# Kernel tuning notes

Measured on AMD Instinct MI355X. Metric: run time of the kernel, lower is better.

Reference implementation:

```python
import jax, jax.numpy as jnp
import numpy as np

N_USERS = 200000
N_ITEMS = 200000
HOPS = 4      # n_hops + 1
DIM = 64
BATCH = 2048
N_NEGS = 64
K = 2
DECAY = 1e-4


def setup_inputs() -> dict:
    key = jax.random.key(0)
    k1, k2, k3, k4, k5, k6 = jax.random.split(key, 6)
    return {
        "user_gcn_emb": jax.random.normal(k1, (N_USERS, HOPS, DIM), dtype=jnp.float32),
        "item_gcn_emb": jax.random.normal(k2, (N_ITEMS, HOPS, DIM), dtype=jnp.float32),
        "seed_embed": jax.random.normal(k3, (BATCH, 1), dtype=jnp.float32),
        "user": jax.random.randint(k4, (BATCH,), 0, N_USERS, dtype=jnp.int64 if jax.config.jax_enable_x64 else jnp.int32),
        "pos_item": jax.random.randint(k5, (BATCH,), 0, N_ITEMS, dtype=jnp.int64 if jax.config.jax_enable_x64 else jnp.int32),
        "neg_item": jax.random.randint(k6, (BATCH, K * N_NEGS), 0, N_ITEMS, dtype=jnp.int64 if jax.config.jax_enable_x64 else jnp.int32),
    }


def _negative_sampling(user_gcn_emb, item_gcn_emb, user, neg_candidates, pos_item, seed_embed):
    # s_e, p_e: [B, H, C]; n_e: [B, N, H, C]
    s_e = user_gcn_emb[user]
    p_e = item_gcn_emb[pos_item]
    n_e = item_gcn_emb[neg_candidates]
    seed = seed_embed[:, :, None, None]                      # [B,1,1,1]
    # positive mixing
    n_e_ = seed * p_e[:, None, :, :] + (1.0 - seed) * n_e    # [B,N,H,C]
    # hop mixing: per-hop inner product scores
    scores = jnp.einsum("bhc,bnhc->bnh", s_e, n_e_)          # [B,N,H]
    idx = jnp.argmax(scores, axis=1)                         # [B,H] (detached/int)
    # select per-hop hardest mixed negative
    sel = jnp.take_along_axis(n_e_, idx[:, None, :, None], axis=1)  # [B,1,H,C]
    return sel[:, 0]                                         # [B,H,C]


def _bpr_loss(user_e, pos_e_hops, neg_e_hops):
    # user_e/pos_e_hops: [B,H,C]; neg_e_hops: [B,K,H,C]
    B = user_e.shape[0]
    u_e = jnp.mean(user_e, axis=1)          # [B,C]  (pool='mean')
    pos_e = jnp.mean(pos_e_hops, axis=1)    # [B,C]
    neg_e = jnp.mean(neg_e_hops, axis=2)    # [B,K,C]
    pos_scores = jnp.sum(u_e * pos_e, axis=-1)              # [B]
    neg_scores = jnp.einsum("bc,bkc->bk", u_e, neg_e)       # [B,K]
    mf_loss = jnp.mean(jnp.log1p(jnp.sum(jnp.exp(neg_scores - pos_scores[:, None]), axis=1)))
    regularize = (jnp.sum(u_e ** 2) + jnp.sum(pos_e ** 2) + jnp.sum(neg_e ** 2)) / 2.0
    emb_loss = DECAY * regularize / B
    return mf_loss + emb_loss, mf_loss, emb_loss


def reference(user_gcn_emb, item_gcn_emb, seed_embed, user, pos_item, neg_item):
    negs = []
    for k in range(K):
        negs.append(_negative_sampling(
            user_gcn_emb, item_gcn_emb, user,
            neg_item[:, k * N_NEGS:(k + 1) * N_NEGS], pos_item, seed_embed))
    neg_gcn_embs = jnp.stack(negs, axis=1)  # [B,K,H,C]
    loss, mf_loss, emb_loss = _bpr_loss(user_gcn_emb[user], item_gcn_emb[pos_item], neg_gcn_embs)
    return loss, mf_loss, emb_loss
```

## Files before the change

kernel.cpp:

```cpp
#include <hip/hip_runtime.h>
#include <math.h>

#define N_USERS 200000
#define N_ITEMS 200000
#define HOPS 4
#define DIM 64
#define BATCH 2048
#define N_NEGS 64
#define KK 2
#define ROW 256
#define DECAY 0.0001f

__global__ __launch_bounds__(256, 4) void mixgcf_main(
    const float* __restrict__ user_emb,
    const float* __restrict__ item_emb,
    const float* __restrict__ seed_embed,
    const int*   __restrict__ user,
    const int*   __restrict__ pos_item,
    const int*   __restrict__ neg_item,
    float*       __restrict__ ws)
{
    const int b    = blockIdx.x;
    const int tid  = threadIdx.x;
    const int w    = tid >> 6;
    const int lane = tid & 63;

    __shared__ float s_lds[ROW];
    __shared__ float p_lds[ROW];
    __shared__ int   nidx[KK * N_NEGS];
    __shared__ float selv[KK][ROW];
    __shared__ float scw[4][HOPS];

    const int   uidx = user[b];
    const int   pidx = pos_item[b];
    const float seed = seed_embed[b];

    if (tid < 64) {
        ((float4*)s_lds)[tid] = *(const float4*)(user_emb + (size_t)uidx * ROW + tid * 4);
    } else if (tid < 128) {
        ((float4*)p_lds)[tid - 64] = *(const float4*)(item_emb + (size_t)pidx * ROW + (tid - 64) * 4);
    } else {
        nidx[tid - 128] = neg_item[(size_t)b * (KK * N_NEGS) + (tid - 128)];
    }
    __syncthreads();

    const float4 s4 = *(const float4*)(s_lds + lane * 4);
    const float4 p4 = *(const float4*)(p_lds + lane * 4);
    const float  omse = 1.0f - seed;
    const float4 sp = make_float4(seed * p4.x, seed * p4.y, seed * p4.z, seed * p4.w);
    const int h = lane >> 4;

    for (int k = 0; k < KK; ++k) {
        float  best = -INFINITY;
        float4 bv   = make_float4(0.f, 0.f, 0.f, 0.f);

        #pragma unroll 4
        for (int i = 0; i < 16; ++i) {
            const int n  = (i << 2) + w;
            const int it = nidx[k * N_NEGS + n];
            const float4 ne = *(const float4*)(item_emb + (size_t)it * ROW + lane * 4);
            float4 ne_;
            ne_.x = fmaf(omse, ne.x, sp.x);
            ne_.y = fmaf(omse, ne.y, sp.y);
            ne_.z = fmaf(omse, ne.z, sp.z);
            ne_.w = fmaf(omse, ne.w, sp.w);
            float sc = ne_.x * s4.x;
            sc = fmaf(ne_.y, s4.y, sc);
            sc = fmaf(ne_.z, s4.z, sc);
            sc = fmaf(ne_.w, s4.w, sc);
            sc += __shfl_xor(sc, 1);
            sc += __shfl_xor(sc, 2);
            sc += __shfl_xor(sc, 4);
            sc += __shfl_xor(sc, 8);
            if (sc > best) { best = sc; bv = ne_; }
        }

        if ((lane & 15) == 0) scw[w][h] = best;
        __syncthreads();
        float m0 = scw[0][h], m1 = scw[1][h], m2 = scw[2][h], m3 = scw[3][h];
        int winner = 0; float mb = m0;
        if (m1 > mb) { mb = m1; winner = 1; }
        if (m2 > mb) { mb = m2; winner = 2; }
        if (m3 > mb) { mb = m3; winner = 3; }
        if (w == winner) {
            *(float4*)(&selv[k][lane * 4]) = bv;
        }
        __syncthreads();
    }

    if (w == 0) {
        const int c = lane;
        const float ue = 0.25f * (s_lds[c] + s_lds[64 + c] + s_lds[128 + c] + s_lds[192 + c]);
        const float pe = 0.25f * (p_lds[c] + p_lds[64 + c] + p_lds[128 + c] + p_lds[192 + c]);
        const float n0 = 0.25f * (selv[0][c] + selv[0][64 + c] + selv[0][128 + c] + selv[0][192 + c]);
        const float n1 = 0.25f * (selv[1][c] + selv[1][64 + c] + selv[1][128 + c] + selv[1][192 + c]);
        float ps  = ue * pe;
        float ns0 = ue * n0;
        float ns1 = ue * n1;
        float rg  = ue * ue + pe * pe + n0 * n0 + n1 * n1;
        #pragma unroll
        for (int m = 1; m < 64; m <<= 1) {
            ps  += __shfl_xor(ps,  m);
            ns0 += __shfl_xor(ns0, m);
            ns1 += __shfl_xor(ns1, m);
            rg  += __shfl_xor(rg,  m);
        }
        if (lane == 0) {
            const float mf = log1pf(expf(ns0 - ps) + expf(ns1 - ps));
            ws[b]         = mf;
            ws[BATCH + b] = rg;
        }
    }
}

__global__ __launch_bounds__(256) void mixgcf_reduce(const float* __restrict__ ws,
                                                     float* __restrict__ out)
{
    __shared__ float smf[256];
    __shared__ float srg[256];
    const int t = threadIdx.x;
    float mf = 0.f, rg = 0.f;
    for (int i = t; i < BATCH; i += 256) {
        mf += ws[i];
        rg += ws[BATCH + i];
    }
    smf[t] = mf; srg[t] = rg;
    __syncthreads();
    for (int s = 128; s > 0; s >>= 1) {
        if (t < s) { smf[t] += smf[t + s]; srg[t] += srg[t + s]; }
        __syncthreads();
    }
    if (t == 0) {
        const float mf_loss  = smf[0] / (float)BATCH;
        const float emb_loss = DECAY * (srg[0] * 0.5f) / (float)BATCH;
        out[0] = mf_loss + emb_loss;
        out[1] = mf_loss;
        out[2] = emb_loss;
    }
}

extern "C" void kernel_launch(void* const* d_in, const int* in_sizes, int n_in,
                              void* d_out, int out_size, void* d_ws, size_t ws_size,
                              hipStream_t stream)
{
    const float* user_emb  = (const float*)d_in[0];
    const float* item_emb  = (const float*)d_in[1];
    const float* seed      = (const float*)d_in[2];
    const int*   user      = (const int*)d_in[3];
    const int*   pos_item  = (const int*)d_in[4];
    const int*   neg_item  = (const int*)d_in[5];
    float* ws  = (float*)d_ws;
    float* out = (float*)d_out;

    mixgcf_main<<<BATCH, 256, 0, stream>>>(user_emb, item_emb, seed,
                                           user, pos_item, neg_item, ws);
    mixgcf_reduce<<<1, 256, 0, stream>>>(ws, out);
}
```

Before: 50.16 us.

## Fuse final reduction via last-block atomic and interleave both negative groups

The separate reduce kernel is folded into the main kernel: each block bumps an atomic counter, and the last block to finish sums the per-sample partials and writes the losses. A memset resets the counter before each launch. The two K negative groups are now processed in one loop, which issues twice as many independent gathers per iteration and removes a pair of barriers. The user and positive rows are loaded straight from global memory rather than staged through LDS. The cost is an extra memset call plus atomic and fence overhead in every block.

```diff
diff --git a/kernel.cpp b/kernel.cpp
--- a/kernel.cpp
+++ b/kernel.cpp
@@ -11,6 +11,8 @@
 #define ROW 256
 #define DECAY 0.0001f
 
+#define WS_OFF 16
+
 __global__ __launch_bounds__(256, 4) void mixgcf_main(
     const float* __restrict__ user_emb,
     const float* __restrict__ item_emb,
@@ -18,80 +20,91 @@
     const int*   __restrict__ user,
     const int*   __restrict__ pos_item,
     const int*   __restrict__ neg_item,
-    float*       __restrict__ ws)
+    float*       __restrict__ ws,
+    float*       __restrict__ out)
 {
     const int b    = blockIdx.x;
     const int tid  = threadIdx.x;
     const int w    = tid >> 6;
     const int lane = tid & 63;
 
-    __shared__ float s_lds[ROW];
-    __shared__ float p_lds[ROW];
     __shared__ int   nidx[KK * N_NEGS];
     __shared__ float selv[KK][ROW];
-    __shared__ float scw[4][HOPS];
+    __shared__ float scw[KK][4][HOPS];
+    __shared__ float red_mf[256];
+    __shared__ float red_rg[256];
+    __shared__ int   last_flag;
 
     const int   uidx = user[b];
     const int   pidx = pos_item[b];
     const float seed = seed_embed[b];
 
-    if (tid < 64) {
-        ((float4*)s_lds)[tid] = *(const float4*)(user_emb + (size_t)uidx * ROW + tid * 4);
-    } else if (tid < 128) {
-        ((float4*)p_lds)[tid - 64] = *(const float4*)(item_emb + (size_t)pidx * ROW + (tid - 64) * 4);
-    } else {
-        nidx[tid - 128] = neg_item[(size_t)b * (KK * N_NEGS) + (tid - 128)];
-    }
+    if (tid < KK * N_NEGS) nidx[tid] = neg_item[(size_t)b * (KK * N_NEGS) + tid];
     __syncthreads();
 
-    const float4 s4 = *(const float4*)(s_lds + lane * 4);
-    const float4 p4 = *(const float4*)(p_lds + lane * 4);
+    const float4 s4 = *(const float4*)(user_emb + (size_t)uidx * ROW + lane * 4);
+    const float4 p4 = *(const float4*)(item_emb + (size_t)pidx * ROW + lane * 4);
     const float  omse = 1.0f - seed;
     const float4 sp = make_float4(seed * p4.x, seed * p4.y, seed * p4.z, seed * p4.w);
     const int h = lane >> 4;
 
-    for (int k = 0; k < KK; ++k) {
-        float  best = -INFINITY;
-        float4 bv   = make_float4(0.f, 0.f, 0.f, 0.f);
+    float  best0 = -INFINITY, best1 = -INFINITY;
+    float4 bv0 = make_float4(0.f, 0.f, 0.f, 0.f);
+    float4 bv1 = make_float4(0.f, 0.f, 0.f, 0.f);
 
-        #pragma unroll 4
-        for (int i = 0; i < 16; ++i) {
-            const int n  = (i << 2) + w;
-            const int it = nidx[k * N_NEGS + n];
-            const float4 ne = *(const float4*)(item_emb + (size_t)it * ROW + lane * 4);
-            float4 ne_;
-            ne_.x = fmaf(omse, ne.x, sp.x);
-            ne_.y = fmaf(omse, ne.y, sp.y);
-            ne_.z = fmaf(omse, ne.z, sp.z);
-            ne_.w = fmaf(omse, ne.w, sp.w);
-            float sc = ne_.x * s4.x;
-            sc = fmaf(ne_.y, s4.y, sc);
-            sc = fmaf(ne_.z, s4.z, sc);
-            sc = fmaf(ne_.w, s4.w, sc);
-            sc += __shfl_xor(sc, 1);
-            sc += __shfl_xor(sc, 2);
-            sc += __shfl_xor(sc, 4);
-            sc += __shfl_xor(sc, 8);
-            if (sc > best) { best = sc; bv = ne_; }
-        }
+    #pragma unroll 8
+    for (int i = 0; i < 16; ++i) {
+        const int n   = (i << 2) + w;
+        const int it0 = nidx[n];
+        const int it1 = nidx[N_NEGS + n];
+        const float4 ne0 = *(const float4*)(item_emb + (size_t)it0 * ROW + lane * 4);
+        const float4 ne1 = *(const float4*)(item_emb + (size_t)it1 * ROW + lane * 4);
 
-        if ((lane & 15) == 0) scw[w][h] = best;
-        __syncthreads();
-        float m0 = scw[0][h], m1 = scw[1][h], m2 = scw[2][h], m3 = scw[3][h];
-        int winner = 0; float mb = m0;
-        if (m1 > mb) { mb = m1; winner = 1; }
-        if (m2 > mb) { mb = m2; winner = 2; }
-        if (m3 > mb) { mb = m3; winner = 3; }
-        if (w == winner) {
-            *(float4*)(&selv[k][lane * 4]) = bv;
-        }
-        __syncthreads();
+        float4 m0, m1;
+        m0.x = fmaf(omse, ne0.x, sp.x); m1.x = fmaf(omse, ne1.x, sp.x);
+        m0.y = fmaf(omse, ne0.y, sp.y); m1.y = fmaf(omse, ne1.y, sp.y);
+        m0.z = fmaf(omse, ne0.z, sp.z); m1.z = fmaf(omse, ne1.z, sp.z);
+        m0.w = fmaf(omse, ne0.w, sp.w); m1.w = fmaf(omse, ne1.w, sp.w);
+
+        float sc0 = m0.x * s4.x;  float sc1 = m1.x * s4.x;
+        sc0 = fmaf(m0.y, s4.y, sc0); sc1 = fmaf(m1.y, s4.y, sc1);
+        sc0 = fmaf(m0.z, s4.z, sc0); sc1 = fmaf(m1.z, s4.z, sc1);
+        sc0 = fmaf(m0.w, s4.w, sc0); sc1 = fmaf(m1.w, s4.w, sc1);
+
+        sc0 += __shfl_xor(sc0, 1);  sc1 += __shfl_xor(sc1, 1);
+        sc0 += __shfl_xor(sc0, 2);  sc1 += __shfl_xor(sc1, 2);
+        sc0 += __shfl_xor(sc0, 4);  sc1 += __shfl_xor(sc1, 4);
+        sc0 += __shfl_xor(sc0, 8);  sc1 += __shfl_xor(sc1, 8);
+
+        if (sc0 > best0) { best0 = sc0; bv0 = m0; }
+        if (sc1 > best1) { best1 = sc1; bv1 = m1; }
     }
+
+    if ((lane & 15) == 0) { scw[0][w][h] = best0; scw[1][w][h] = best1; }
+    __syncthreads();
+    {
+        float a0 = scw[0][0][h], a1 = scw[0][1][h], a2 = scw[0][2][h], a3 = scw[0][3][h];
+        int win0 = 0; float mb = a0;
+        if (a1 > mb) { mb = a1; win0 = 1; }
+        if (a2 > mb) { mb = a2; win0 = 2; }
+        if (a3 > mb) { mb = a3; win0 = 3; }
+        if (w == win0) *(float4*)(&selv[0][lane * 4]) = bv0;
+
+        float c0 = scw[1][0][h], c1 = scw[1][1][h], c2 = scw[1][2][h], c3 = scw[1][3][h];
+        int win1 = 0; float nb = c0;
+        if (c1 > nb) { nb = c1; win1 = 1; }
+        if (c2 > nb) { nb = c2; win1 = 2; }
+        if (c3 > nb) { nb = c3; win1 = 3; }
+        if (w == win1) *(float4*)(&selv[1][lane * 4]) = bv1;
+    }
+    __syncthreads();
 
     if (w == 0) {
         const int c = lane;
-        const float ue = 0.25f * (s_lds[c] + s_lds[64 + c] + s_lds[128 + c] + s_lds[192 + c]);
-        const float pe = 0.25f * (p_lds[c] + p_lds[64 + c] + p_lds[128 + c] + p_lds[192 + c]);
+        const float* ur = user_emb + (size_t)uidx * ROW;
+        const float* pr = item_emb + (size_t)pidx * ROW;
+        const float ue = 0.25f * (ur[c] + ur[64 + c] + ur[128 + c] + ur[192 + c]);
+        const float pe = 0.25f * (pr[c] + pr[64 + c] + pr[128 + c] + pr[192 + c]);
         const float n0 = 0.25f * (selv[0][c] + selv[0][64 + c] + selv[0][128 + c] + selv[0][192 + c]);
         const float n1 = 0.25f * (selv[1][c] + selv[1][64 + c] + selv[1][128 + c] + selv[1][192 + c]);
         float ps  = ue * pe;
@@ -107,35 +120,37 @@
         }
         if (lane == 0) {
             const float mf = log1pf(expf(ns0 - ps) + expf(ns1 - ps));
-            ws[b]         = mf;
-            ws[BATCH + b] = rg;
+            ws[WS_OFF + b]         = mf;
+            ws[WS_OFF + BATCH + b] = rg;
         }
     }
-}
 
-__global__ __launch_bounds__(256) void mixgcf_reduce(const float* __restrict__ ws,
-                                                     float* __restrict__ out)
-{
-    __shared__ float smf[256];
-    __shared__ float srg[256];
-    const int t = threadIdx.x;
-    float mf = 0.f, rg = 0.f;
-    for (int i = t; i < BATCH; i += 256) {
-        mf += ws[i];
-        rg += ws[BATCH + i];
+    if (tid == 0) {
+        __threadfence();
+        unsigned t = atomicAdd((unsigned*)ws, 1u);
+        last_flag = (t == (unsigned)(BATCH - 1));
     }
-    smf[t] = mf; srg[t] = rg;
     __syncthreads();
-    for (int s = 128; s > 0; s >>= 1) {
-        if (t < s) { smf[t] += smf[t + s]; srg[t] += srg[t + s]; }
+    if (last_flag) {
+        __threadfence();
+        float mf = 0.f, rg = 0.f;
+        for (int i = tid; i < BATCH; i += 256) {
+            mf += ws[WS_OFF + i];
+            rg += ws[WS_OFF + BATCH + i];
+        }
+        red_mf[tid] = mf; red_rg[tid] = rg;
         __syncthreads();
-    }
-    if (t == 0) {
-        const float mf_loss  = smf[0] / (float)BATCH;
-        const float emb_loss = DECAY * (srg[0] * 0.5f) / (float)BATCH;
-        out[0] = mf_loss + emb_loss;
-        out[1] = mf_loss;
-        out[2] = emb_loss;
+        for (int s = 128; s > 0; s >>= 1) {
+            if (tid < s) { red_mf[tid] += red_mf[tid + s]; red_rg[tid] += red_rg[tid + s]; }
+            __syncthreads();
+        }
+        if (tid == 0) {
+            const float mf_loss  = red_mf[0] / (float)BATCH;
+            const float emb_loss = DECAY * (red_rg[0] * 0.5f) / (float)BATCH;
+            out[0] = mf_loss + emb_loss;
+            out[1] = mf_loss;
+            out[2] = emb_loss;
+        }
     }
 }
 
@@ -152,7 +167,7 @@
     float* ws  = (float*)d_ws;
     float* out = (float*)d_out;
 
+    hipMemsetAsync(d_ws, 0, 4, stream);
     mixgcf_main<<<BATCH, 256, 0, stream>>>(user_emb, item_emb, seed,
-                                           user, pos_item, neg_item, ws);
-    mixgcf_reduce<<<1, 256, 0, stream>>>(ws, out);
+                                           user, pos_item, neg_item, ws, out);
 }
```

After: 115.5 us. +130.3%, slower.
